# Optimization experiments

Measured on AMD Instinct MI355X. Metric: run time of the kernel, lower is better.

Reference implementation:

```python
import jax, jax.numpy as jnp
import numpy as np

FPFM = 256.0
B = 2097152
C = 32


def _integerize(v, scale):
    # Mirrors ArmInt.set_param_from_float: round-half-away-from-zero to int,
    # stored back as float (pure_int=False path).
    fv = v * scale
    fv = fv + jnp.sign(fv) * 0.5
    return jnp.trunc(fv)  # trunc toward zero == torch .to(int32)


def setup_inputs() -> dict:
    key = jax.random.key(0)
    ks = jax.random.split(key, 8)
    x = jax.random.normal(ks[0], (B, C), dtype=jnp.float32)
    # float-domain params (small, residual-friendly), then integerized
    w0 = _integerize(jax.random.normal(ks[1], (C, C), jnp.float32) * 0.05, FPFM)
    b0 = _integerize(jax.random.normal(ks[2], (C,), jnp.float32) * 0.05, FPFM * FPFM)
    w1 = _integerize(jax.random.normal(ks[3], (C, C), jnp.float32) * 0.05, FPFM)
    b1 = _integerize(jax.random.normal(ks[4], (C,), jnp.float32) * 0.05, FPFM * FPFM)
    w_out = _integerize(jax.random.normal(ks[5], (2, C), jnp.float32) * 0.05, FPFM)
    b_out = _integerize(jax.random.normal(ks[6], (2,), jnp.float32) * 0.05, FPFM * FPFM)
    return {"x": x, "w0": w0, "b0": b0, "w1": w1, "b1": b1,
            "w_out": w_out, "b_out": b_out}


def _arm_layer(h, W, b, residual):
    # F.linear + optional residual scaled by FPFM
    xx = h @ W.T + b
    if residual:
        xx = xx + h * FPFM
    # emulated integer rounding: add sign*FPFM/2, divide, trunc toward zero
    xx = xx + jnp.sign(xx) * (FPFM / 2.0)
    # where(xx<0, -(-xx/f), xx/f) is identity in float; trunc matches .to(int32)
    return jnp.trunc(xx / FPFM)


def reference(x, w0, b0, w1, b1, w_out, b_out):
    h = x * FPFM  # fixed-point lift (pure_int=False: stays float)
    h = jax.nn.relu(_arm_layer(h, w0, b0, True))
    h = jax.nn.relu(_arm_layer(h, w1, b1, True))
    h = _arm_layer(h, w_out, b_out, False)
    raw = h / FPFM  # [B, 2]
    mu = raw[:, 0]
    log_scale = raw[:, 1]
    scale = jnp.exp(jnp.clip(log_scale - 4.0, -4.6, 5.0))
    return mu, scale, log_scale
```

## Files before the change

### kernel.cpp

```cpp
#include <hip/hip_runtime.h>
#include <math.h>


typedef __attribute__((ext_vector_type(8))) short bf16x8;
typedef __attribute__((ext_vector_type(4))) float f32x4;

#define MFMA16(A, B, C) __builtin_amdgcn_mfma_f32_16x16x32_bf16((A), (B), (C), 0, 0, 0)

__device__ inline short bf_top(float v) {
    return (short)(__float_as_uint(v) >> 16);
}
__device__ inline float bf_topf(float v) {
    return __uint_as_float(__float_as_uint(v) & 0xffff0000u);
}


__global__ void armint_prep(const float* __restrict__ w0, const float* __restrict__ b0,
                            const float* __restrict__ w1, const float* __restrict__ b1,
                            const float* __restrict__ wo, const float* __restrict__ bo,
                            short* __restrict__ ws, float* __restrict__ bsf)
{
    int t = threadIdx.x;
    for (int i = t; i < 1024; i += 256) {
        int n = i >> 5, k = i & 31;
        float diag = (n == k) ? 256.0f : 0.0f;

        float a = w0[i] + diag;
        float ahi = bf_topf(a);
        ws[i]          = bf_top(a);
        ws[1024 + i]   = bf_top(a - ahi);

        float b = (w1[i] + diag) * (1.0f / 256.0f);
        float bhi = bf_topf(b);
        ws[2048 + i]   = bf_top(b);
        ws[3072 + i]   = bf_top(b - bhi);

        float c = (n < 2) ? wo[n * 32 + k] * (1.0f / 256.0f) : 0.0f;
        ws[4096 + i]   = bf_top(c);
    }
    if (t < 32) {
        bsf[t]      = (b0[t] + 128.0f) * (1.0f / 256.0f);
        bsf[32 + t] = (b1[t] + 128.0f) * (1.0f / 256.0f);
        bsf[64 + t] = (t < 2) ? bo[t] * (1.0f / 256.0f) : 0.0f;
    }
}

__global__ __launch_bounds__(256)
void armint_mfma(const float* __restrict__ x, const short* __restrict__ ws,
                 const float* __restrict__ bias, float* __restrict__ out, int nrows)
{
    __shared__ float lds_all[4][32 * 36];

    const int lane = threadIdx.x & 63;
    const int wave = threadIdx.x >> 6;
    const int lm   = lane & 15;
    const int quad = lane >> 4;
    float* lds = lds_all[wave];

    const size_t nn = (size_t)nrows;
    const size_t rowbase = (size_t)blockIdx.x * 128 + (size_t)wave * 32;

    bf16x8 w0hi[2], w0lo[2], w1hi[2], w1lo[2], wof;
    float bs0[2], bs1[2];
    #pragma unroll
    for (int hh = 0; hh < 2; ++hh) {
        const int n = lm + 16 * hh;
        const int o = n * 32 + quad * 8;
        w0hi[hh] = *(const bf16x8*)(ws + o);
        w0lo[hh] = *(const bf16x8*)(ws + 1024 + o);
        w1hi[hh] = *(const bf16x8*)(ws + 2048 + o);
        w1lo[hh] = *(const bf16x8*)(ws + 3072 + o);
        bs0[hh] = bias[n];
        bs1[hh] = bias[32 + n];
    }
    wof = *(const bf16x8*)(ws + 4096 + lm * 32 + quad * 8);
    const float bsov = bias[64 + lm];

    bf16x8 a0[2], a1[2], a2[2];
    #pragma unroll
    for (int t = 0; t < 2; ++t) {
        const float* xp = x + (rowbase + (size_t)(t * 16 + lm)) * 32 + quad * 8;
        float4 v0 = *(const float4*)xp;
        float4 v1 = *(const float4*)(xp + 4);
        float h[8] = {v0.x, v0.y, v0.z, v0.w, v1.x, v1.y, v1.z, v1.w};
        #pragma unroll
        for (int j = 0; j < 8; ++j) {
            float c0 = bf_topf(h[j]);
            a0[t][j] = bf_top(h[j]);
            float r1 = h[j] - c0;
            float c1 = bf_topf(r1);
            a1[t][j] = bf_top(r1);
            a2[t][j] = bf_top(r1 - c1);
        }
    }

    f32x4 acc[2][2];
    #pragma unroll
    for (int t = 0; t < 2; ++t)
        #pragma unroll
        for (int hh = 0; hh < 2; ++hh) {
            f32x4 c = {bs0[hh], bs0[hh], bs0[hh], bs0[hh]};
            c = MFMA16(a0[t], w0hi[hh], c);
            c = MFMA16(a1[t], w0hi[hh], c);
            c = MFMA16(a2[t], w0hi[hh], c);
            c = MFMA16(a0[t], w0lo[hh], c);
            c = MFMA16(a1[t], w0lo[hh], c);
            acc[t][hh] = c;
        }
    #pragma unroll
    for (int t = 0; t < 2; ++t)
        #pragma unroll
        for (int hh = 0; hh < 2; ++hh)
            #pragma unroll
            for (int k = 0; k < 4; ++k)
                lds[(t * 16 + quad * 4 + k) * 36 + lm + 16 * hh] =
                    fmaxf(truncf(acc[t][hh][k]), 0.0f);

    bf16x8 c0f[2], c1f[2];
    #pragma unroll
    for (int t = 0; t < 2; ++t) {
        const int base = (t * 16 + lm) * 36 + quad * 8;
        float4 v0 = *(float4*)&lds[base];
        float4 v1 = *(float4*)&lds[base + 4];
        float h[8] = {v0.x, v0.y, v0.z, v0.w, v1.x, v1.y, v1.z, v1.w};
        #pragma unroll
        for (int j = 0; j < 8; ++j) {
            float c0 = bf_topf(h[j]);
            c0f[t][j] = bf_top(h[j]);
            c1f[t][j] = bf_top(h[j] - c0);
        }
    }
    #pragma unroll
    for (int t = 0; t < 2; ++t)
        #pragma unroll
        for (int hh = 0; hh < 2; ++hh) {
            f32x4 c = {bs1[hh], bs1[hh], bs1[hh], bs1[hh]};
            c = MFMA16(c0f[t], w1hi[hh], c);
            c = MFMA16(c1f[t], w1hi[hh], c);
            c = MFMA16(c0f[t], w1lo[hh], c);
            c = MFMA16(c1f[t], w1lo[hh], c);
            acc[t][hh] = c;
        }
    #pragma unroll
    for (int t = 0; t < 2; ++t)
        #pragma unroll
        for (int hh = 0; hh < 2; ++hh)
            #pragma unroll
            for (int k = 0; k < 4; ++k)
                lds[(t * 16 + quad * 4 + k) * 36 + lm + 16 * hh] =
                    fmaxf(truncf(acc[t][hh][k]), 0.0f);

    bf16x8 d0f[2], d1f[2];
    #pragma unroll
    for (int t = 0; t < 2; ++t) {
        const int base = (t * 16 + lm) * 36 + quad * 8;
        float4 v0 = *(float4*)&lds[base];
        float4 v1 = *(float4*)&lds[base + 4];
        float h[8] = {v0.x, v0.y, v0.z, v0.w, v1.x, v1.y, v1.z, v1.w};
        #pragma unroll
        for (int j = 0; j < 8; ++j) {
            float c0 = bf_topf(h[j]);
            d0f[t][j] = bf_top(h[j]);
            d1f[t][j] = bf_top(h[j] - c0);
        }
    }
    #pragma unroll
    for (int t = 0; t < 2; ++t) {
        f32x4 c = {bsov, bsov, bsov, bsov};
        c = MFMA16(d0f[t], wof, c);
        c = MFMA16(d1f[t], wof, c);

        float o[4];
        #pragma unroll
        for (int k = 0; k < 4; ++k) {
            float a = c[k];
            o[k] = truncf(a + copysignf(0.5f, a)) * (1.0f / 256.0f);
        }
        const size_t row = rowbase + (size_t)(t * 16 + quad * 4);
        if (lm == 0) {
            *(float4*)(out + row) = make_float4(o[0], o[1], o[2], o[3]);
        }
        if (lm == 1) {
            *(float4*)(out + 2 * nn + row) = make_float4(o[0], o[1], o[2], o[3]);
            float s[4];
            #pragma unroll
            for (int k = 0; k < 4; ++k)
                s[k] = expf(fminf(fmaxf(o[k] - 4.0f, -4.6f), 5.0f));
            *(float4*)(out + nn + row) = make_float4(s[0], s[1], s[2], s[3]);
        }
    }
}

extern "C" void kernel_launch(void* const* d_in, const int* in_sizes, int n_in,
                              void* d_out, int out_size, void* d_ws, size_t ws_size,
                              hipStream_t stream) {
    const float* x  = (const float*)d_in[0];
    const float* w0 = (const float*)d_in[1];
    const float* b0 = (const float*)d_in[2];
    const float* w1 = (const float*)d_in[3];
    const float* b1 = (const float*)d_in[4];
    const float* wo = (const float*)d_in[5];
    const float* bo = (const float*)d_in[6];
    float* out = (float*)d_out;

    short* ws  = (short*)d_ws;
    float* bsf = (float*)((char*)d_ws + 10240);

    int nrows = in_sizes[0] / 32;
    int grid = nrows / 128;

    armint_prep<<<1, 256, 0, stream>>>(w0, b0, w1, b1, wo, bo, ws, bsf);
    armint_mfma<<<grid, 256, 0, stream>>>(x, ws, bsf, out, nrows);
}
```

Before: 371.0 us.

## Replace LDS transposes with transposed MFMA and permlane swaps; compute output layer in FP32

Swaps the MFMA operand order so each layer's output lands transposed, then uses v_permlane32/16_swap to rebuild the next layer's A-operand in registers instead of writing to and reading back from LDS. The final 2-output layer becomes an FP32 dot product reduced across lanes with permlane swaps, replacing the bf16 MFMA. This removes the LDS round-trips and the shared-memory allocation. In exchange it relies on gfx950-specific permlane swap instructions and adds per-lane ALU work for the last layer.

```diff
diff --git a/kernel.cpp b/kernel.cpp
--- a/kernel.cpp
+++ b/kernel.cpp
@@ -14,10 +14,16 @@
     return __uint_as_float(__float_as_uint(v) & 0xffff0000u);
 }
 
+__device__ inline void pl32swap(float& a, float& b) {
+    asm("v_permlane32_swap_b32 %0, %1" : "+v"(a), "+v"(b));
+}
+__device__ inline void pl16swap(float& a, float& b) {
+    asm("v_permlane16_swap_b32 %0, %1" : "+v"(a), "+v"(b));
+}
+
 
 __global__ void armint_prep(const float* __restrict__ w0, const float* __restrict__ b0,
                             const float* __restrict__ w1, const float* __restrict__ b1,
-                            const float* __restrict__ wo, const float* __restrict__ bo,
                             short* __restrict__ ws, float* __restrict__ bsf)
 {
     int t = threadIdx.x;
@@ -34,47 +40,43 @@
         float bhi = bf_topf(b);
         ws[2048 + i]   = bf_top(b);
         ws[3072 + i]   = bf_top(b - bhi);
-
-        float c = (n < 2) ? wo[n * 32 + k] * (1.0f / 256.0f) : 0.0f;
-        ws[4096 + i]   = bf_top(c);
     }
     if (t < 32) {
         bsf[t]      = (b0[t] + 128.0f) * (1.0f / 256.0f);
         bsf[32 + t] = (b1[t] + 128.0f) * (1.0f / 256.0f);
-        bsf[64 + t] = (t < 2) ? bo[t] * (1.0f / 256.0f) : 0.0f;
     }
 }
 
 __global__ __launch_bounds__(256)
 void armint_mfma(const float* __restrict__ x, const short* __restrict__ ws,
-                 const float* __restrict__ bias, float* __restrict__ out, int nrows)
+                 const float* __restrict__ bias, const float* __restrict__ wo,
+                 const float* __restrict__ bo, float* __restrict__ out, int nrows)
 {
-    __shared__ float lds_all[4][32 * 36];
-
     const int lane = threadIdx.x & 63;
     const int wave = threadIdx.x >> 6;
     const int lm   = lane & 15;
     const int quad = lane >> 4;
-    float* lds = lds_all[wave];
 
     const size_t nn = (size_t)nrows;
     const size_t rowbase = (size_t)blockIdx.x * 128 + (size_t)wave * 32;
 
-    bf16x8 w0hi[2], w0lo[2], w1hi[2], w1lo[2], wof;
-    float bs0[2], bs1[2];
+    bf16x8 w0hi[2], w0lo[2], w1hi[2], w1lo[2];
     #pragma unroll
     for (int hh = 0; hh < 2; ++hh) {
-        const int n = lm + 16 * hh;
-        const int o = n * 32 + quad * 8;
+        const int o = (lm + 16 * hh) * 32 + quad * 8;
         w0hi[hh] = *(const bf16x8*)(ws + o);
         w0lo[hh] = *(const bf16x8*)(ws + 1024 + o);
         w1hi[hh] = *(const bf16x8*)(ws + 2048 + o);
         w1lo[hh] = *(const bf16x8*)(ws + 3072 + o);
-        bs0[hh] = bias[n];
-        bs1[hh] = bias[32 + n];
-    }
-    wof = *(const bf16x8*)(ws + 4096 + lm * 32 + quad * 8);
-    const float bsov = bias[64 + lm];
+    }
+    f32x4 bv0[2], bv1[2];
+    #pragma unroll
+    for (int hh = 0; hh < 2; ++hh) {
+        float4 t0 = *(const float4*)(bias + hh * 16 + quad * 4);
+        float4 t1 = *(const float4*)(bias + 32 + hh * 16 + quad * 4);
+        bv0[hh][0] = t0.x; bv0[hh][1] = t0.y; bv0[hh][2] = t0.z; bv0[hh][3] = t0.w;
+        bv1[hh][0] = t1.x; bv1[hh][1] = t1.y; bv1[hh][2] = t1.z; bv1[hh][3] = t1.w;
+    }
 
     bf16x8 a0[2], a1[2], a2[2];
     #pragma unroll
@@ -99,94 +101,84 @@
     for (int t = 0; t < 2; ++t)
         #pragma unroll
         for (int hh = 0; hh < 2; ++hh) {
-            f32x4 c = {bs0[hh], bs0[hh], bs0[hh], bs0[hh]};
-            c = MFMA16(a0[t], w0hi[hh], c);
-            c = MFMA16(a1[t], w0hi[hh], c);
-            c = MFMA16(a2[t], w0hi[hh], c);
-            c = MFMA16(a0[t], w0lo[hh], c);
-            c = MFMA16(a1[t], w0lo[hh], c);
+            f32x4 c = bv0[hh];
+            c = MFMA16(w0hi[hh], a0[t], c);
+            c = MFMA16(w0hi[hh], a1[t], c);
+            c = MFMA16(w0hi[hh], a2[t], c);
+            c = MFMA16(w0lo[hh], a0[t], c);
+            c = MFMA16(w0lo[hh], a1[t], c);
             acc[t][hh] = c;
         }
+
+    bf16x8 c0f[2], c1f[2];
+    #pragma unroll
+    for (int t = 0; t < 2; ++t) {
+        float X0[4], X1[4];
+        #pragma unroll
+        for (int r = 0; r < 4; ++r) {
+            X0[r] = fmaxf(truncf(acc[t][0][r]), 0.0f);
+            X1[r] = fmaxf(truncf(acc[t][1][r]), 0.0f);
+            pl32swap(X0[r], X1[r]);
+            pl16swap(X0[r], X1[r]);
+        }
+        #pragma unroll
+        for (int j = 0; j < 8; ++j) {
+            float v = (j < 4) ? X0[j] : X1[j - 4];
+            float hi = bf_topf(v);
+            c0f[t][j] = bf_top(v);
+            c1f[t][j] = bf_top(v - hi);
+        }
+    }
+
     #pragma unroll
     for (int t = 0; t < 2; ++t)
         #pragma unroll
-        for (int hh = 0; hh < 2; ++hh)
-            #pragma unroll
-            for (int k = 0; k < 4; ++k)
-                lds[(t * 16 + quad * 4 + k) * 36 + lm + 16 * hh] =
-                    fmaxf(truncf(acc[t][hh][k]), 0.0f);
-
-    bf16x8 c0f[2], c1f[2];
+        for (int hh = 0; hh < 2; ++hh) {
+            f32x4 c = bv1[hh];
+            c = MFMA16(w1hi[hh], c0f[t], c);
+            c = MFMA16(w1hi[hh], c1f[t], c);
+            c = MFMA16(w1lo[hh], c0f[t], c);
+            c = MFMA16(w1lo[hh], c1f[t], c);
+            acc[t][hh] = c;
+        }
+
+    float wlo[2][4], whi[2][4];
+    #pragma unroll
+    for (int o = 0; o < 2; ++o) {
+        float4 va = *(const float4*)(wo + o * 32 + quad * 4);
+        float4 vb = *(const float4*)(wo + o * 32 + 16 + quad * 4);
+        wlo[o][0] = va.x; wlo[o][1] = va.y; wlo[o][2] = va.z; wlo[o][3] = va.w;
+        whi[o][0] = vb.x; whi[o][1] = vb.y; whi[o][2] = vb.z; whi[o][3] = vb.w;
+    }
+    const float bo0 = bo[0], bo1 = bo[1];
+
     #pragma unroll
     for (int t = 0; t < 2; ++t) {
-        const int base = (t * 16 + lm) * 36 + quad * 8;
-        float4 v0 = *(float4*)&lds[base];
-        float4 v1 = *(float4*)&lds[base + 4];
-        float h[8] = {v0.x, v0.y, v0.z, v0.w, v1.x, v1.y, v1.z, v1.w};
-        #pragma unroll
-        for (int j = 0; j < 8; ++j) {
-            float c0 = bf_topf(h[j]);
-            c0f[t][j] = bf_top(h[j]);
-            c1f[t][j] = bf_top(h[j] - c0);
-        }
-    }
-    #pragma unroll
-    for (int t = 0; t < 2; ++t)
-        #pragma unroll
-        for (int hh = 0; hh < 2; ++hh) {
-            f32x4 c = {bs1[hh], bs1[hh], bs1[hh], bs1[hh]};
-            c = MFMA16(c0f[t], w1hi[hh], c);
-            c = MFMA16(c1f[t], w1hi[hh], c);
-            c = MFMA16(c0f[t], w1lo[hh], c);
-            c = MFMA16(c1f[t], w1lo[hh], c);
-            acc[t][hh] = c;
-        }
-    #pragma unroll
-    for (int t = 0; t < 2; ++t)
-        #pragma unroll
-        for (int hh = 0; hh < 2; ++hh)
-            #pragma unroll
-            for (int k = 0; k < 4; ++k)
-                lds[(t * 16 + quad * 4 + k) * 36 + lm + 16 * hh] =
-                    fmaxf(truncf(acc[t][hh][k]), 0.0f);
-
-    bf16x8 d0f[2], d1f[2];
-    #pragma unroll
-    for (int t = 0; t < 2; ++t) {
-        const int base = (t * 16 + lm) * 36 + quad * 8;
-        float4 v0 = *(float4*)&lds[base];
-        float4 v1 = *(float4*)&lds[base + 4];
-        float h[8] = {v0.x, v0.y, v0.z, v0.w, v1.x, v1.y, v1.z, v1.w};
-        #pragma unroll
-        for (int j = 0; j < 8; ++j) {
-            float c0 = bf_topf(h[j]);
-            d0f[t][j] = bf_top(h[j]);
-            d1f[t][j] = bf_top(h[j] - c0);
-        }
-    }
-    #pragma unroll
-    for (int t = 0; t < 2; ++t) {
-        f32x4 c = {bsov, bsov, bsov, bsov};
-        c = MFMA16(d0f[t], wof, c);
-        c = MFMA16(d1f[t], wof, c);
-
-        float o[4];
-        #pragma unroll
-        for (int k = 0; k < 4; ++k) {
-            float a = c[k];
-            o[k] = truncf(a + copysignf(0.5f, a)) * (1.0f / 256.0f);
-        }
-        const size_t row = rowbase + (size_t)(t * 16 + quad * 4);
-        if (lm == 0) {
-            *(float4*)(out + row) = make_float4(o[0], o[1], o[2], o[3]);
-        }
-        if (lm == 1) {
-            *(float4*)(out + 2 * nn + row) = make_float4(o[0], o[1], o[2], o[3]);
-            float s[4];
-            #pragma unroll
-            for (int k = 0; k < 4; ++k)
-                s[k] = expf(fminf(fmaxf(o[k] - 4.0f, -4.6f), 5.0f));
-            *(float4*)(out + nn + row) = make_float4(s[0], s[1], s[2], s[3]);
+        float p0 = 0.0f, p1 = 0.0f;
+        #pragma unroll
+        for (int r = 0; r < 4; ++r) {
+            float g0 = fmaxf(truncf(acc[t][0][r]), 0.0f);
+            float g1 = fmaxf(truncf(acc[t][1][r]), 0.0f);
+            p0 += g0 * wlo[0][r] + g1 * whi[0][r];
+            p1 += g0 * wlo[1][r] + g1 * whi[1][r];
+        }
+        float u0 = p0, u1 = p1;
+        pl32swap(p0, u0); p0 += u0;
+        pl32swap(p1, u1); p1 += u1;
+        float v0 = p0, v1 = p1;
+        pl16swap(p0, v0); p0 += v0;
+        pl16swap(p1, v1); p1 += v1;
+
+        if (quad == 0) {
+            const size_t row = rowbase + (size_t)(t * 16 + lm);
+            float amu = (p0 + bo0) * (1.0f / 256.0f);
+            float omu = truncf(amu + copysignf(0.5f, amu)) * (1.0f / 256.0f);
+            float als = (p1 + bo1) * (1.0f / 256.0f);
+            float ols = truncf(als + copysignf(0.5f, als)) * (1.0f / 256.0f);
+            float sc  = expf(fminf(fmaxf(ols - 4.0f, -4.6f), 5.0f));
+            out[row]          = omu;
+            out[nn + row]     = sc;
+            out[2 * nn + row] = ols;
         }
     }
 }
@@ -204,11 +196,11 @@
     float* out = (float*)d_out;
 
     short* ws  = (short*)d_ws;
-    float* bsf = (float*)((char*)d_ws + 10240);
+    float* bsf = (float*)((char*)d_ws + 8192);
 
     int nrows = in_sizes[0] / 32;
     int grid = nrows / 128;
 
-    armint_prep<<<1, 256, 0, stream>>>(w0, b0, w1, b1, wo, bo, ws, bsf);
-    armint_mfma<<<grid, 256, 0, stream>>>(x, ws, bsf, out, nrows);
-}
+    armint_prep<<<1, 256, 0, stream>>>(w0, b0, w1, b1, ws, bsf);
+    armint_mfma<<<grid, 256, 0, stream>>>(x, ws, bsf, wo, bo, out, nrows);
+}
```

After: 373.1 us. About the same (+0.6%).
